# Kernel optimization log

Measured on AMD Instinct MI355X. Metric: run time of the kernel, lower is better.

## Reference

```python
import jax, jax.numpy as jnp
import numpy as np

POOL = 7           # pool_size_after_rpn
CROP = POOL * 2    # pre_pool_size


def _crop_resize_pool(bottom, rois, im_info):
    # TF tf.image.crop_and_resize (bilinear, extrapolation_value=0) fused with 2x2 max pool
    B, H, W, C = bottom.shape
    dt = bottom.dtype
    batch_ids = rois[:, 0].astype(jnp.int32)            # [N]
    im_h, im_w = im_info[0], im_info[1]
    x1 = rois[:, 1] / im_w
    y1 = rois[:, 2] / im_h
    x2 = rois[:, 3] / im_w
    y2 = rois[:, 4] / im_h
    grid = jnp.arange(CROP, dtype=dt)
    # TF sampling grid for crop_size>1: in_y = y1*(H-1) + i*(y2-y1)*(H-1)/(crop-1)
    ys = y1[:, None] * (H - 1) + grid[None, :] * ((y2 - y1) * (H - 1) / (CROP - 1))[:, None]  # [N,ch]
    xs = x1[:, None] * (W - 1) + grid[None, :] * ((x2 - x1) * (W - 1) / (CROP - 1))[:, None]  # [N,cw]
    vy = (ys >= 0) & (ys <= H - 1)
    vx = (xs >= 0) & (xs <= W - 1)
    y0f = jnp.floor(ys)
    x0f = jnp.floor(xs)
    ly = (ys - y0f)[:, :, None, None]                   # [N,ch,1,1]
    lx = (xs - x0f)[:, None, :, None]                   # [N,1,cw,1]
    y0 = jnp.clip(y0f, 0, H - 1).astype(jnp.int32)
    y1i = jnp.clip(jnp.ceil(ys), 0, H - 1).astype(jnp.int32)
    x0 = jnp.clip(x0f, 0, W - 1).astype(jnp.int32)
    x1i = jnp.clip(jnp.ceil(xs), 0, W - 1).astype(jnp.int32)
    flat = bottom.reshape(B * H * W, C)
    base = (batch_ids * (H * W))[:, None, None]

    def g(yi, xi):
        # irregular per-box gather of corner values -> [N,ch,cw,C]
        return jnp.take(flat, base + yi[:, :, None] * W + xi[:, None, :], axis=0)

    tl, tr, bl, br = g(y0, x0), g(y0, x1i), g(y1i, x0), g(y1i, x1i)
    top = tl + (tr - tl) * lx
    bot = bl + (br - bl) * lx
    crops = top + (bot - top) * ly                      # [N,CROP,CROP,C]
    mask = (vy[:, :, None] & vx[:, None, :])[..., None]
    crops = jnp.where(mask, crops, jnp.zeros((), dt))   # extrapolation_value = 0
    N = crops.shape[0]
    # MaxPooling2D(pool_size=2, strides=2, padding='SAME'); CROP is even -> exact 2x2 blocks
    return crops.reshape(N, POOL, 2, POOL, 2, C).max(axis=(2, 4))


def setup_inputs() -> dict:
    key = jax.random.key(0)
    kb, k0, k1, k2, k3 = jax.random.split(key, 5)
    B, H, W, C, NROI = 2, 64, 64, 512, 512
    IM = 1024.0
    bottom = jax.random.normal(kb, (B, H, W, C), dtype=jnp.float32)
    bids = jax.random.randint(k0, (NROI,), 0, B).astype(jnp.float32)
    x1 = jax.random.uniform(k1, (NROI,), minval=0.0, maxval=IM - 64.0)
    y1 = jax.random.uniform(k2, (NROI,), minval=0.0, maxval=IM - 64.0)
    wh = jax.random.uniform(k3, (NROI, 2), minval=32.0, maxval=256.0)
    x2 = jnp.minimum(x1 + wh[:, 0], IM - 1.0)
    y2 = jnp.minimum(y1 + wh[:, 1], IM - 1.0)
    rois = jnp.stack([bids, x1, y1, x2, y2], axis=1)    # [N,5]: (batch_id,x1,y1,x2,y2)
    im_info = jnp.array([IM, IM], dtype=jnp.float32)    # [height, width]
    return {"bottom": bottom, "rois": rois, "im_info": im_info}


def reference(bottom, rois, im_info):
    return _crop_resize_pool(bottom, rois, im_info)
```

## Files before the change

kernel.cpp:

```cpp
#include <hip/hip_runtime.h>
#include <math.h>


constexpr int POOLSZ = 7;
constexpr int CROPSZ = 14;
constexpr int Hc = 64, Wc = 64, C4 = 128;

typedef float vfloat4 __attribute__((ext_vector_type(4)));

__device__ __forceinline__ float4 lerp4(float4 a, float4 b, float t) {
    return make_float4(fmaf(b.x - a.x, t, a.x),
                       fmaf(b.y - a.y, t, a.y),
                       fmaf(b.z - a.z, t, a.z),
                       fmaf(b.w - a.w, t, a.w));
}
__device__ __forceinline__ float4 f4max(float4 a, float4 b) {
    return make_float4(fmaxf(a.x, b.x), fmaxf(a.y, b.y),
                       fmaxf(a.z, b.z), fmaxf(a.w, b.w));
}
__device__ __forceinline__ float4 mask4(float4 v, bool ok) {
    return ok ? v : make_float4(0.f, 0.f, 0.f, 0.f);
}
__device__ __forceinline__ int rfl(int x) { return __builtin_amdgcn_readfirstlane(x); }

__global__ __launch_bounds__(128)
void crop_pool_kernel(const float4* __restrict__ bot4,
                      const float* __restrict__ rois,
                      const float* __restrict__ im_info,
                      float4* __restrict__ out4, int nwg)
{
    const int bid = blockIdx.x;
    const int blk = (bid & 7) * (nwg >> 3) + (bid >> 3);

    const int n  = blk / (POOLSZ * POOLSZ);
    const int p  = blk - n * (POOLSZ * POOLSZ);
    const int py = p / POOLSZ;
    const int px = p - py * POOLSZ;

    const float inv_w = 1.0f / im_info[1];
    const float inv_h = 1.0f / im_info[0];
    const float* r5 = rois + n * 5;
    const int bb = rfl((int)r5[0]);
    const float rx1 = r5[1] * inv_w, ry1 = r5[2] * inv_h;
    const float rx2 = r5[3] * inv_w, ry2 = r5[4] * inv_h;

    const float sy = (ry2 - ry1) * (float)(Hc - 1) / (float)(CROPSZ - 1);
    const float sx = (rx2 - rx1) * (float)(Wc - 1) / (float)(CROPSZ - 1);
    const float oy = ry1 * (float)(Hc - 1);
    const float ox = rx1 * (float)(Wc - 1);

    int R0, R1, R2, R3;
    float ly0, ly1; bool vy0, vy1;
    {
        const float ysa = fmaf((float)(2 * py), sy, oy);
        vy0 = (ysa >= 0.f) && (ysa <= (float)(Hc - 1));
        const float fy = floorf(ysa); ly0 = ysa - fy;
        const int y0 = (int)fminf(fmaxf(fy, 0.f), (float)(Hc - 1));
        const int y1 = (int)fminf(fmaxf(ceilf(ysa), 0.f), (float)(Hc - 1));
        R0 = rfl(((bb * Hc + y0) * Wc) * C4);
        R1 = rfl(((bb * Hc + y1) * Wc) * C4);
        const float ysb = fmaf((float)(2 * py + 1), sy, oy);
        vy1 = (ysb >= 0.f) && (ysb <= (float)(Hc - 1));
        const float fy2 = floorf(ysb); ly1 = ysb - fy2;
        const int y2 = (int)fminf(fmaxf(fy2, 0.f), (float)(Hc - 1));
        const int y3 = (int)fminf(fmaxf(ceilf(ysb), 0.f), (float)(Hc - 1));
        R2 = rfl(((bb * Hc + y2) * Wc) * C4);
        R3 = rfl(((bb * Hc + y3) * Wc) * C4);
    }
    int cA, cB, cC, cD;
    float lx0, lx1; bool vx0, vx1;
    {
        const float xsa = fmaf((float)(2 * px), sx, ox);
        vx0 = (xsa >= 0.f) && (xsa <= (float)(Wc - 1));
        const float fx = floorf(xsa); lx0 = xsa - fx;
        cA = rfl((int)fminf(fmaxf(fx, 0.f), (float)(Wc - 1)) * C4);
        cB = rfl((int)fminf(fmaxf(ceilf(xsa), 0.f), (float)(Wc - 1)) * C4);
        const float xsb = fmaf((float)(2 * px + 1), sx, ox);
        vx1 = (xsb >= 0.f) && (xsb <= (float)(Wc - 1));
        const float fx2 = floorf(xsb); lx1 = xsb - fx2;
        cC = rfl((int)fminf(fmaxf(fx2, 0.f), (float)(Wc - 1)) * C4);
        cD = rfl((int)fminf(fmaxf(ceilf(xsb), 0.f), (float)(Wc - 1)) * C4);
    }

    const int tid = threadIdx.x;

    float4 X00, X01, X10, X11, X20, X21, X30, X31;

    auto fresh = [&](int rb, float4& Xs0, float4& Xs1) {
        const float4 a = bot4[rb + cA + tid];
        float4 b; if (cB != cA) b = bot4[rb + cB + tid]; else b = a;
        float4 c; if (cC == cA) c = a; else if (cC == cB) c = b;
                  else c = bot4[rb + cC + tid];
        float4 d; if (cD == cC) d = c; else if (cD == cB) d = b;
                  else d = bot4[rb + cD + tid];
        Xs0 = lerp4(a, b, lx0);
        Xs1 = lerp4(c, d, lx1);
    };

    fresh(R0, X00, X01);
    if (R1 == R0)      { X10 = X00; X11 = X01; }
    else                 fresh(R1, X10, X11);
    if (R2 == R0)      { X20 = X00; X21 = X01; }
    else if (R2 == R1) { X20 = X10; X21 = X11; }
    else                 fresh(R2, X20, X21);
    if (R3 == R2)      { X30 = X20; X31 = X21; }
    else if (R3 == R1) { X30 = X10; X31 = X11; }
    else                 fresh(R3, X30, X31);

    const float4 v00 = lerp4(X00, X10, ly0);
    const float4 v01 = lerp4(X01, X11, ly0);
    const float4 v10 = lerp4(X20, X30, ly1);
    const float4 v11 = lerp4(X21, X31, ly1);

    const float4 acc = f4max(
        f4max(mask4(v00, vy0 && vx0), mask4(v01, vy0 && vx1)),
        f4max(mask4(v10, vy1 && vx0), mask4(v11, vy1 && vx1)));

    vfloat4 accv; accv.x = acc.x; accv.y = acc.y; accv.z = acc.z; accv.w = acc.w;
    vfloat4* dst = reinterpret_cast<vfloat4*>(&out4[(size_t)blk * C4 + tid]);
    __builtin_nontemporal_store(accv, dst);
}

extern "C" void kernel_launch(void* const* d_in, const int* in_sizes, int n_in,
                              void* d_out, int out_size, void* d_ws, size_t ws_size,
                              hipStream_t stream) {
    const float4* bottom  = (const float4*)d_in[0];
    const float*  rois    = (const float*)d_in[1];
    const float*  im_info = (const float*)d_in[2];
    float4* out = (float4*)d_out;

    const int N = in_sizes[1] / 5;
    const int nwg = N * POOLSZ * POOLSZ;

    crop_pool_kernel<<<nwg, 128, 0, stream>>>(bottom, rois, im_info, out, nwg);
}
```

Baseline: 31.58 us.

## Precompute per-cell sampling geometry in a separate kernel before gather

```diff
diff --git a/kernel.cpp b/kernel.cpp
--- a/kernel.cpp
+++ b/kernel.cpp
@@ -5,6 +5,7 @@
 constexpr int POOLSZ = 7;
 constexpr int CROPSZ = 14;
 constexpr int Hc = 64, Wc = 64, C4 = 128;
+constexpr int NCELLS_WORDS = 16;
 
 typedef float vfloat4 __attribute__((ext_vector_type(4)));
 
@@ -23,15 +24,132 @@
 }
 __device__ __forceinline__ int rfl(int x) { return __builtin_amdgcn_readfirstlane(x); }
 
+__global__ __launch_bounds__(256)
+void geom_kernel(const float* __restrict__ rois,
+                 const float* __restrict__ im_info,
+                 int* __restrict__ gout, int ncells)
+{
+    const int cell = blockIdx.x * 256 + threadIdx.x;
+    if (cell >= ncells) return;
+    const int n  = cell / (POOLSZ * POOLSZ);
+    const int p  = cell - n * (POOLSZ * POOLSZ);
+    const int py = p / POOLSZ;
+    const int px = p - py * POOLSZ;
+
+    const float inv_w = 1.0f / im_info[1];
+    const float inv_h = 1.0f / im_info[0];
+    const float* r5 = rois + n * 5;
+    const int bb = (int)r5[0];
+    const float rx1 = r5[1] * inv_w, ry1 = r5[2] * inv_h;
+    const float rx2 = r5[3] * inv_w, ry2 = r5[4] * inv_h;
+
+    const float sy = (ry2 - ry1) * (float)(Hc - 1) / (float)(CROPSZ - 1);
+    const float sx = (rx2 - rx1) * (float)(Wc - 1) / (float)(CROPSZ - 1);
+    const float oy = ry1 * (float)(Hc - 1);
+    const float ox = rx1 * (float)(Wc - 1);
+
+    int g[NCELLS_WORDS];
+    const float ysa = fmaf((float)(2 * py), sy, oy);
+    const bool vy0 = (ysa >= 0.f) && (ysa <= (float)(Hc - 1));
+    const float fy = floorf(ysa); const float ly0 = ysa - fy;
+    const int y0 = (int)fminf(fmaxf(fy, 0.f), (float)(Hc - 1));
+    const int y1 = (int)fminf(fmaxf(ceilf(ysa), 0.f), (float)(Hc - 1));
+    g[0] = ((bb * Hc + y0) * Wc) * C4;
+    g[1] = ((bb * Hc + y1) * Wc) * C4;
+    const float ysb = fmaf((float)(2 * py + 1), sy, oy);
+    const bool vy1 = (ysb >= 0.f) && (ysb <= (float)(Hc - 1));
+    const float fy2 = floorf(ysb); const float ly1 = ysb - fy2;
+    const int y2 = (int)fminf(fmaxf(fy2, 0.f), (float)(Hc - 1));
+    const int y3 = (int)fminf(fmaxf(ceilf(ysb), 0.f), (float)(Hc - 1));
+    g[2] = ((bb * Hc + y2) * Wc) * C4;
+    g[3] = ((bb * Hc + y3) * Wc) * C4;
+    const float xsa = fmaf((float)(2 * px), sx, ox);
+    const bool vx0 = (xsa >= 0.f) && (xsa <= (float)(Wc - 1));
+    const float fx = floorf(xsa); const float lx0 = xsa - fx;
+    g[4] = (int)fminf(fmaxf(fx, 0.f), (float)(Wc - 1)) * C4;
+    g[5] = (int)fminf(fmaxf(ceilf(xsa), 0.f), (float)(Wc - 1)) * C4;
+    const float xsb = fmaf((float)(2 * px + 1), sx, ox);
+    const bool vx1 = (xsb >= 0.f) && (xsb <= (float)(Wc - 1));
+    const float fx2 = floorf(xsb); const float lx1 = xsb - fx2;
+    g[6] = (int)fminf(fmaxf(fx2, 0.f), (float)(Wc - 1)) * C4;
+    g[7] = (int)fminf(fmaxf(ceilf(xsb), 0.f), (float)(Wc - 1)) * C4;
+    g[8]  = __float_as_int(lx0);
+    g[9]  = __float_as_int(lx1);
+    g[10] = __float_as_int(ly0);
+    g[11] = __float_as_int(ly1);
+    g[12] = (int)((vy0 && vx0) ? 1u : 0u) | ((vy0 && vx1) ? 2u : 0u)
+          | ((vy1 && vx0) ? 4u : 0u) | ((vy1 && vx1) ? 8u : 0u);
+    g[13] = g[14] = g[15] = 0;
+
+    int4* dst = reinterpret_cast<int4*>(gout + (size_t)cell * NCELLS_WORDS);
+    int4* s = reinterpret_cast<int4*>(g);
+    dst[0] = s[0]; dst[1] = s[1]; dst[2] = s[2]; dst[3] = s[3];
+}
+
 __global__ __launch_bounds__(128)
 void crop_pool_kernel(const float4* __restrict__ bot4,
-                      const float* __restrict__ rois,
-                      const float* __restrict__ im_info,
+                      const int* __restrict__ geom,
                       float4* __restrict__ out4, int nwg)
 {
     const int bid = blockIdx.x;
     const int blk = (bid & 7) * (nwg >> 3) + (bid >> 3);
 
+    const int* g = geom + (size_t)blk * NCELLS_WORDS;
+    const int R0 = rfl(g[0]), R1 = rfl(g[1]), R2 = rfl(g[2]), R3 = rfl(g[3]);
+    const int cA = rfl(g[4]), cB = rfl(g[5]), cC = rfl(g[6]), cD = rfl(g[7]);
+    const float lx0 = __int_as_float(rfl(g[8]));
+    const float lx1 = __int_as_float(rfl(g[9]));
+    const float ly0 = __int_as_float(rfl(g[10]));
+    const float ly1 = __int_as_float(rfl(g[11]));
+    const int msk = rfl(g[12]);
+
+    const int tid = threadIdx.x;
+
+    float4 X00, X01, X10, X11, X20, X21, X30, X31;
+    auto fresh = [&](int rb, float4& Xs0, float4& Xs1) {
+        const float4 a = bot4[rb + cA + tid];
+        float4 b; if (cB != cA) b = bot4[rb + cB + tid]; else b = a;
+        float4 c; if (cC == cA) c = a; else if (cC == cB) c = b;
+                  else c = bot4[rb + cC + tid];
+        float4 d; if (cD == cC) d = c; else if (cD == cB) d = b;
+                  else d = bot4[rb + cD + tid];
+        Xs0 = lerp4(a, b, lx0);
+        Xs1 = lerp4(c, d, lx1);
+    };
+
+    fresh(R0, X00, X01);
+    if (R1 == R0)      { X10 = X00; X11 = X01; }
+    else                 fresh(R1, X10, X11);
+    if (R2 == R0)      { X20 = X00; X21 = X01; }
+    else if (R2 == R1) { X20 = X10; X21 = X11; }
+    else                 fresh(R2, X20, X21);
+    if (R3 == R2)      { X30 = X20; X31 = X21; }
+    else if (R3 == R1) { X30 = X10; X31 = X11; }
+    else                 fresh(R3, X30, X31);
+
+    const float4 v00 = lerp4(X00, X10, ly0);
+    const float4 v01 = lerp4(X01, X11, ly0);
+    const float4 v10 = lerp4(X20, X30, ly1);
+    const float4 v11 = lerp4(X21, X31, ly1);
+
+    const float4 acc = f4max(
+        f4max(mask4(v00, (msk & 1) != 0), mask4(v01, (msk & 2) != 0)),
+        f4max(mask4(v10, (msk & 4) != 0), mask4(v11, (msk & 8) != 0)));
+
+    vfloat4 accv; accv.x = acc.x; accv.y = acc.y; accv.z = acc.z; accv.w = acc.w;
+    vfloat4* dst = reinterpret_cast<vfloat4*>(
+        const_cast<float4*>(&out4[(size_t)blk * C4 + tid]));
+    __builtin_nontemporal_store(accv, dst);
+}
+
+__global__ __launch_bounds__(128)
+void crop_pool_mono(const float4* __restrict__ bot4,
+                    const float* __restrict__ rois,
+                    const float* __restrict__ im_info,
+                    float4* __restrict__ out4, int nwg)
+{
+    const int bid = blockIdx.x;
+    const int blk = (bid & 7) * (nwg >> 3) + (bid >> 3);
     const int n  = blk / (POOLSZ * POOLSZ);
     const int p  = blk - n * (POOLSZ * POOLSZ);
     const int py = p / POOLSZ;
@@ -43,14 +161,12 @@
     const int bb = rfl((int)r5[0]);
     const float rx1 = r5[1] * inv_w, ry1 = r5[2] * inv_h;
     const float rx2 = r5[3] * inv_w, ry2 = r5[4] * inv_h;
-
     const float sy = (ry2 - ry1) * (float)(Hc - 1) / (float)(CROPSZ - 1);
     const float sx = (rx2 - rx1) * (float)(Wc - 1) / (float)(CROPSZ - 1);
     const float oy = ry1 * (float)(Hc - 1);
     const float ox = rx1 * (float)(Wc - 1);
 
-    int R0, R1, R2, R3;
-    float ly0, ly1; bool vy0, vy1;
+    int R0, R1, R2, R3; float ly0, ly1; bool vy0, vy1;
     {
         const float ysa = fmaf((float)(2 * py), sy, oy);
         vy0 = (ysa >= 0.f) && (ysa <= (float)(Hc - 1));
@@ -67,8 +183,7 @@
         R2 = rfl(((bb * Hc + y2) * Wc) * C4);
         R3 = rfl(((bb * Hc + y3) * Wc) * C4);
     }
-    int cA, cB, cC, cD;
-    float lx0, lx1; bool vx0, vx1;
+    int cA, cB, cC, cD; float lx0, lx1; bool vx0, vx1;
     {
         const float xsa = fmaf((float)(2 * px), sx, ox);
         vx0 = (xsa >= 0.f) && (xsa <= (float)(Wc - 1));
@@ -81,11 +196,8 @@
         cC = rfl((int)fminf(fmaxf(fx2, 0.f), (float)(Wc - 1)) * C4);
         cD = rfl((int)fminf(fmaxf(ceilf(xsb), 0.f), (float)(Wc - 1)) * C4);
     }
-
     const int tid = threadIdx.x;
-
     float4 X00, X01, X10, X11, X20, X21, X30, X31;
-
     auto fresh = [&](int rb, float4& Xs0, float4& Xs1) {
         const float4 a = bot4[rb + cA + tid];
         float4 b; if (cB != cA) b = bot4[rb + cB + tid]; else b = a;
@@ -96,7 +208,6 @@
         Xs0 = lerp4(a, b, lx0);
         Xs1 = lerp4(c, d, lx1);
     };
-
     fresh(R0, X00, X01);
     if (R1 == R0)      { X10 = X00; X11 = X01; }
     else                 fresh(R1, X10, X11);
@@ -106,19 +217,16 @@
     if (R3 == R2)      { X30 = X20; X31 = X21; }
     else if (R3 == R1) { X30 = X10; X31 = X11; }
     else                 fresh(R3, X30, X31);
-
     const float4 v00 = lerp4(X00, X10, ly0);
     const float4 v01 = lerp4(X01, X11, ly0);
     const float4 v10 = lerp4(X20, X30, ly1);
     const float4 v11 = lerp4(X21, X31, ly1);
-
     const float4 acc = f4max(
         f4max(mask4(v00, vy0 && vx0), mask4(v01, vy0 && vx1)),
         f4max(mask4(v10, vy1 && vx0), mask4(v11, vy1 && vx1)));
-
     vfloat4 accv; accv.x = acc.x; accv.y = acc.y; accv.z = acc.z; accv.w = acc.w;
-    vfloat4* dst = reinterpret_cast<vfloat4*>(&out4[(size_t)blk * C4 + tid]);
-    __builtin_nontemporal_store(accv, dst);
+    __builtin_nontemporal_store(accv,
+        reinterpret_cast<vfloat4*>(&out4[(size_t)blk * C4 + tid]));
 }
 
 extern "C" void kernel_launch(void* const* d_in, const int* in_sizes, int n_in,
@@ -132,5 +240,12 @@
     const int N = in_sizes[1] / 5;
     const int nwg = N * POOLSZ * POOLSZ;
 
-    crop_pool_kernel<<<nwg, 128, 0, stream>>>(bottom, rois, im_info, out, nwg);
-}
+    const size_t need = (size_t)nwg * NCELLS_WORDS * sizeof(int);
+    if (ws_size >= need) {
+        int* geom = (int*)d_ws;
+        geom_kernel<<<(nwg + 255) / 256, 256, 0, stream>>>(rois, im_info, geom, nwg);
+        crop_pool_kernel<<<nwg, 128, 0, stream>>>(bottom, geom, out, nwg);
+    } else {
+        crop_pool_mono<<<nwg, 128, 0, stream>>>(bottom, rois, im_info, out, nwg);
+    }
+}
```

New measurement: 34.74 us. +10.0%, slower.
